# Performance work log

Measured on AMD Instinct MI355X. Metric: run time of the kernel, lower is better.

The kernel has to match this reference:

```python
import jax, jax.numpy as jnp
import numpy as np

S, I, H = 4096, 2048, 2048


def setup_inputs() -> dict:
    key = jax.random.key(0)
    ks = jax.random.split(key, 7)
    k = 1.0 / np.sqrt(H)  # torch LSTMCell init range (values don't affect math shape)
    x = jax.random.normal(ks[0], (S, I), dtype=jnp.float32)
    W_ih = jax.random.uniform(ks[1], (4 * H, I), minval=-k, maxval=k, dtype=jnp.float32)
    W_hh = jax.random.uniform(ks[2], (4 * H, H), minval=-k, maxval=k, dtype=jnp.float32)
    b_ih = jax.random.uniform(ks[3], (4 * H,), minval=-k, maxval=k, dtype=jnp.float32)
    b_hh = jax.random.uniform(ks[4], (4 * H,), minval=-k, maxval=k, dtype=jnp.float32)
    xav = np.sqrt(2.0 / (1 + H))  # xavier_normal_ std for a (1, H) tensor
    h0 = jax.random.normal(ks[5], (1, H), dtype=jnp.float32) * xav
    c0 = jax.random.normal(ks[6], (1, H), dtype=jnp.float32) * xav
    return {"x": x, "W_ih": W_ih, "W_hh": W_hh, "b_ih": b_ih, "b_hh": b_hh, "h0": h0, "c0": c0}


def reference(x, W_ih, W_hh, b_ih, b_hh, h0, c0):
    # Precompute input contribution for all timesteps in one big GEMM: (S, 4H)
    x_gates = x @ W_ih.T + b_ih + b_hh
    W_hh_T = W_hh.T  # (H, 4H)

    def step(carry, xg_t):
        h, c = carry  # each (H,)
        gates = xg_t + h @ W_hh_T  # (4H,)
        i, f, g, o = jnp.split(gates, 4)
        i = jax.nn.sigmoid(i)
        f = jax.nn.sigmoid(f)
        g = jnp.tanh(g)
        o = jax.nn.sigmoid(o)
        c_new = f * c + i * g
        h_new = o * jnp.tanh(c_new)
        return (h_new, c_new), h_new

    _, hs = jax.lax.scan(step, (h0[0], c0[0]), x_gates)
    return hs[:, None, :]  # (S, 1, H) matching torch.stack of (1, H) states
```

## Files before the change

kernel.cpp:

```cpp
#include <hip/hip_runtime.h>
#include <hip/hip_bf16.h>

#define S_LEN 4096
#define IDIM  2048
#define HDIM  2048
#define G4    8192
#define NB    256
#define TPB   512

__device__ __forceinline__ unsigned short f2bf(float f) {
  unsigned u = __float_as_uint(f);
  unsigned r = (u + 0x7FFFu + ((u >> 16) & 1u)) >> 16;
  return (unsigned short)r;
}
__device__ __forceinline__ float bf2f(unsigned short h) {
  return __uint_as_float(((unsigned)h) << 16);
}

__device__ __forceinline__ unsigned long long pack_rec(float h, unsigned tag) {
  return (unsigned long long)__float_as_uint(h) | ((unsigned long long)tag << 32);
}

#define TS 64
#define KS 16
__global__ __launch_bounds__(256) void gemm_xg(
    const float* __restrict__ x, const float* __restrict__ Wih,
    const float* __restrict__ bih, const float* __restrict__ bhh,
    unsigned short* __restrict__ xg) {
  __shared__ float At[KS][TS + 4];
  __shared__ float Bt[KS][TS + 4];
  const int t  = threadIdx.x;
  const int tx = t & 15, ty = t >> 4;
  const int s0 = blockIdx.y * TS, j0 = blockIdx.x * TS;
  const int lrow = t >> 2, lk4 = (t & 3) * 4;
  float acc[4][4] = {};

  for (int k0 = 0; k0 < IDIM; k0 += KS) {
    const float4 av = *(const float4*)&x  [(size_t)(s0 + lrow) * IDIM + k0 + lk4];
    const float4 bv = *(const float4*)&Wih[(size_t)(j0 + lrow) * IDIM + k0 + lk4];
    __syncthreads();
    At[lk4+0][lrow] = av.x; At[lk4+1][lrow] = av.y;
    At[lk4+2][lrow] = av.z; At[lk4+3][lrow] = av.w;
    Bt[lk4+0][lrow] = bv.x; Bt[lk4+1][lrow] = bv.y;
    Bt[lk4+2][lrow] = bv.z; Bt[lk4+3][lrow] = bv.w;
    __syncthreads();
#pragma unroll
    for (int k = 0; k < KS; ++k) {
      float a[4], bb[4];
      *(float4*)a  = *(const float4*)&At[k][ty * 4];
      *(float4*)bb = *(const float4*)&Bt[k][tx * 4];
#pragma unroll
      for (int i = 0; i < 4; ++i)
#pragma unroll
        for (int j = 0; j < 4; ++j)
          acc[i][j] = fmaf(a[i], bb[j], acc[i][j]);
    }
  }
  const float4 b1 = *(const float4*)&bih[j0 + tx * 4];
  const float4 b2 = *(const float4*)&bhh[j0 + tx * 4];
  const float bias[4] = {b1.x + b2.x, b1.y + b2.y, b1.z + b2.z, b1.w + b2.w};
#pragma unroll
  for (int i = 0; i < 4; ++i) {
    ushort4 pk;
    pk.x = f2bf(acc[i][0] + bias[0]);
    pk.y = f2bf(acc[i][1] + bias[1]);
    pk.z = f2bf(acc[i][2] + bias[2]);
    pk.w = f2bf(acc[i][3] + bias[3]);
    *(ushort4*)&xg[(size_t)(s0 + ty * 4 + i) * G4 + j0 + tx * 4] = pk;
  }
}

__global__ __launch_bounds__(TPB, 2) void lstm_scan(
    const unsigned short* __restrict__ xg, const float* __restrict__ Whh,
    const float* __restrict__ h0, const float* __restrict__ c0,
    float* __restrict__ out, unsigned long long* __restrict__ rec) {
  __shared__ float h_sh[2][HDIM];
  __shared__ float part[16][33];

  const int b = blockIdx.x, t = threadIdx.x;
  const int r = t & 31, c = t >> 5;
  const size_t row_g = (size_t)(r >> 3) * HDIM + b * 8 + (r & 7);

  float w[128];
  {
    const float* wp = Whh + row_g * HDIM + c * 128;
#pragma unroll
    for (int i = 0; i < 32; ++i) {
      const float4 v = *(const float4*)(wp + i * 4);
      w[i*4+0] = v.x; w[i*4+1] = v.y; w[i*4+2] = v.z; w[i*4+3] = v.w;
    }
  }
  float c_reg = (t < 8) ? c0[b * 8 + t] : 0.f;

  for (int ts = 0; ts < S_LEN; ++ts) {
    const int buf = ts & 1;
    float xgv = 0.f;
    if (t < 32)
      xgv = bf2f(xg[(size_t)ts * G4 + (size_t)(t >> 3) * HDIM + b * 8 + (t & 7)]);

    if (ts == 0) {
      h_sh[0][t]        = h0[t];
      h_sh[0][t + 512]  = h0[t + 512];
      h_sh[0][t + 1024] = h0[t + 1024];
      h_sh[0][t + 1536] = h0[t + 1536];
    } else {
      const unsigned want = (unsigned)ts;
      const unsigned long long* slot = rec + (size_t)(ts & 1) * HDIM;
      unsigned long long r0, r1, r2, r3;
      for (;;) {
        r0 = __hip_atomic_load(slot + t,        __ATOMIC_RELAXED, __HIP_MEMORY_SCOPE_AGENT);
        r1 = __hip_atomic_load(slot + t + 512,  __ATOMIC_RELAXED, __HIP_MEMORY_SCOPE_AGENT);
        r2 = __hip_atomic_load(slot + t + 1024, __ATOMIC_RELAXED, __HIP_MEMORY_SCOPE_AGENT);
        r3 = __hip_atomic_load(slot + t + 1536, __ATOMIC_RELAXED, __HIP_MEMORY_SCOPE_AGENT);
        if ((unsigned)(r0 >> 32) == want && (unsigned)(r1 >> 32) == want &&
            (unsigned)(r2 >> 32) == want && (unsigned)(r3 >> 32) == want)
          break;
        __builtin_amdgcn_s_sleep(2);
      }
      h_sh[buf][t]        = __uint_as_float((unsigned)r0);
      h_sh[buf][t + 512]  = __uint_as_float((unsigned)r1);
      h_sh[buf][t + 1024] = __uint_as_float((unsigned)r2);
      h_sh[buf][t + 1536] = __uint_as_float((unsigned)r3);
    }
    __syncthreads();

    float acc = 0.f;
    const float4* h4 = (const float4*)&h_sh[buf][c * 128];
#pragma unroll
    for (int i = 0; i < 32; ++i) {
      const float4 hv = h4[i];
      acc = fmaf(w[i*4+0], hv.x, acc);
      acc = fmaf(w[i*4+1], hv.y, acc);
      acc = fmaf(w[i*4+2], hv.z, acc);
      acc = fmaf(w[i*4+3], hv.w, acc);
    }
    part[c][r] = acc;
    __syncthreads();

    if (t < 64) {
      float gval = 0.f;
      if (t < 32) {
        float s = xgv;
#pragma unroll
        for (int i = 0; i < 16; ++i) s += part[i][t];
        gval = ((t >> 3) == 2) ? tanhf(s) : 1.f / (1.f + __expf(-s));
      }
      const float iv = __shfl(gval, (t & 7));
      const float fv = __shfl(gval, (t & 7) + 8);
      const float gv = __shfl(gval, (t & 7) + 16);
      const float ov = __shfl(gval, (t & 7) + 24);
      if (t < 8) {
        c_reg = fmaf(fv, c_reg, iv * gv);
        const float hn = ov * tanhf(c_reg);
        const int j = b * 8 + t;
        out[(size_t)ts * HDIM + j] = hn;
        __hip_atomic_store(&rec[(size_t)((ts + 1) & 1) * HDIM + j],
                           pack_rec(hn, (unsigned)(ts + 1)),
                           __ATOMIC_RELAXED, __HIP_MEMORY_SCOPE_AGENT);
      }
    }
  }
}

extern "C" void kernel_launch(void* const* d_in, const int* in_sizes, int n_in,
                              void* d_out, int out_size, void* d_ws, size_t ws_size,
                              hipStream_t stream) {
  const float* x   = (const float*)d_in[0];
  const float* Wih = (const float*)d_in[1];
  const float* Whh = (const float*)d_in[2];
  const float* bih = (const float*)d_in[3];
  const float* bhh = (const float*)d_in[4];
  const float* h0  = (const float*)d_in[5];
  const float* c0  = (const float*)d_in[6];
  float* out = (float*)d_out;

  unsigned long long* rec = (unsigned long long*)d_ws;
  unsigned short* xg = (unsigned short*)((char*)d_ws + 32768);

  hipMemsetAsync(rec, 0, 2 * HDIM * sizeof(unsigned long long), stream);

  dim3 g1(G4 / TS, S_LEN / TS);
  gemm_xg<<<g1, 256, 0, stream>>>(x, Wih, bih, bhh, xg);

  void* args[] = {(void*)&xg, (void*)&Whh, (void*)&h0,
                  (void*)&c0, (void*)&out, (void*)&rec};
  hipLaunchCooperativeKernel((void*)lstm_scan, dim3(NB), dim3(TPB),
                             args, 0, stream);
}
```

Before: 13.41 ms.

## Use bf16 MFMA for input GEMM and warp-per-unit recurrent scan

```diff
diff --git a/kernel.cpp b/kernel.cpp
--- a/kernel.cpp
+++ b/kernel.cpp
@@ -8,6 +8,9 @@
 #define NB    256
 #define TPB   512
 
+typedef __attribute__((ext_vector_type(8))) short     bf16x8;
+typedef __attribute__((ext_vector_type(4))) float     f32x4;
+
 __device__ __forceinline__ unsigned short f2bf(float f) {
   unsigned u = __float_as_uint(f);
   unsigned r = (u + 0x7FFFu + ((u >> 16) & 1u)) >> 16;
@@ -16,57 +19,88 @@
 __device__ __forceinline__ float bf2f(unsigned short h) {
   return __uint_as_float(((unsigned)h) << 16);
 }
-
 __device__ __forceinline__ unsigned long long pack_rec(float h, unsigned tag) {
   return (unsigned long long)__float_as_uint(h) | ((unsigned long long)tag << 32);
 }
 
-#define TS 64
-#define KS 16
-__global__ __launch_bounds__(256) void gemm_xg(
+#define BM 128
+#define BKK 32
+#define LDK 40
+
+__global__ __launch_bounds__(256) void gemm_xg_mfma(
     const float* __restrict__ x, const float* __restrict__ Wih,
     const float* __restrict__ bih, const float* __restrict__ bhh,
     unsigned short* __restrict__ xg) {
-  __shared__ float At[KS][TS + 4];
-  __shared__ float Bt[KS][TS + 4];
-  const int t  = threadIdx.x;
-  const int tx = t & 15, ty = t >> 4;
-  const int s0 = blockIdx.y * TS, j0 = blockIdx.x * TS;
-  const int lrow = t >> 2, lk4 = (t & 3) * 4;
-  float acc[4][4] = {};
-
-  for (int k0 = 0; k0 < IDIM; k0 += KS) {
-    const float4 av = *(const float4*)&x  [(size_t)(s0 + lrow) * IDIM + k0 + lk4];
-    const float4 bv = *(const float4*)&Wih[(size_t)(j0 + lrow) * IDIM + k0 + lk4];
+  __shared__ unsigned short As[BM][LDK];
+  __shared__ unsigned short Bs[BM][LDK];
+
+  const int t = threadIdx.x;
+  const int lane = t & 63, wid = t >> 6;
+  const int wr = wid >> 1, wc = wid & 1;
+
+  int bid = ((int)blockIdx.x & 7) * 256 + ((int)blockIdx.x >> 3);
+  const int s0 = (bid >> 6) * BM;
+  const int j0 = (bid & 63) * BM;
+
+  f32x4 acc[4][4] = {};
+
+  float bias[4];
+#pragma unroll
+  for (int n = 0; n < 4; ++n) {
+    const int col = j0 + wc * 64 + n * 16 + (lane & 15);
+    bias[n] = bih[col] + bhh[col];
+  }
+
+  for (int k0 = 0; k0 < IDIM; k0 += BKK) {
+    float4 va[4], vb[4];
+#pragma unroll
+    for (int u = 0; u < 4; ++u) {
+      const int f = t + 256 * u;
+      const int row = f >> 3, kc = (f & 7) * 4;
+      va[u] = *(const float4*)&x  [(size_t)(s0 + row) * IDIM + k0 + kc];
+      vb[u] = *(const float4*)&Wih[(size_t)(j0 + row) * IDIM + k0 + kc];
+    }
     __syncthreads();
-    At[lk4+0][lrow] = av.x; At[lk4+1][lrow] = av.y;
-    At[lk4+2][lrow] = av.z; At[lk4+3][lrow] = av.w;
-    Bt[lk4+0][lrow] = bv.x; Bt[lk4+1][lrow] = bv.y;
-    Bt[lk4+2][lrow] = bv.z; Bt[lk4+3][lrow] = bv.w;
+#pragma unroll
+    for (int u = 0; u < 4; ++u) {
+      const int f = t + 256 * u;
+      const int row = f >> 3, kc = (f & 7) * 4;
+      ushort4 pa, pb;
+      pa.x = f2bf(va[u].x); pa.y = f2bf(va[u].y);
+      pa.z = f2bf(va[u].z); pa.w = f2bf(va[u].w);
+      pb.x = f2bf(vb[u].x); pb.y = f2bf(vb[u].y);
+      pb.z = f2bf(vb[u].z); pb.w = f2bf(vb[u].w);
+      *(ushort4*)&As[row][kc] = pa;
+      *(ushort4*)&Bs[row][kc] = pb;
+    }
     __syncthreads();
-#pragma unroll
-    for (int k = 0; k < KS; ++k) {
-      float a[4], bb[4];
-      *(float4*)a  = *(const float4*)&At[k][ty * 4];
-      *(float4*)bb = *(const float4*)&Bt[k][tx * 4];
-#pragma unroll
-      for (int i = 0; i < 4; ++i)
-#pragma unroll
-        for (int j = 0; j < 4; ++j)
-          acc[i][j] = fmaf(a[i], bb[j], acc[i][j]);
-    }
-  }
-  const float4 b1 = *(const float4*)&bih[j0 + tx * 4];
-  const float4 b2 = *(const float4*)&bhh[j0 + tx * 4];
-  const float bias[4] = {b1.x + b2.x, b1.y + b2.y, b1.z + b2.z, b1.w + b2.w};
-#pragma unroll
-  for (int i = 0; i < 4; ++i) {
-    ushort4 pk;
-    pk.x = f2bf(acc[i][0] + bias[0]);
-    pk.y = f2bf(acc[i][1] + bias[1]);
-    pk.z = f2bf(acc[i][2] + bias[2]);
-    pk.w = f2bf(acc[i][3] + bias[3]);
-    *(ushort4*)&xg[(size_t)(s0 + ty * 4 + i) * G4 + j0 + tx * 4] = pk;
+
+    const int fr = lane & 15, koff = (lane >> 4) * 8;
+    bf16x8 a[4], bfr[4];
+#pragma unroll
+    for (int m = 0; m < 4; ++m)
+      a[m] = *(const bf16x8*)&As[wr * 64 + m * 16 + fr][koff];
+#pragma unroll
+    for (int n = 0; n < 4; ++n)
+      bfr[n] = *(const bf16x8*)&Bs[wc * 64 + n * 16 + fr][koff];
+#pragma unroll
+    for (int m = 0; m < 4; ++m)
+#pragma unroll
+      for (int n = 0; n < 4; ++n)
+        acc[m][n] = __builtin_amdgcn_mfma_f32_16x16x32_bf16(
+            a[m], bfr[n], acc[m][n], 0, 0, 0);
+  }
+
+#pragma unroll
+  for (int m = 0; m < 4; ++m) {
+    const int row0 = s0 + wr * 64 + m * 16 + (lane >> 4) * 4;
+#pragma unroll
+    for (int n = 0; n < 4; ++n) {
+      const int col = j0 + wc * 64 + n * 16 + (lane & 15);
+#pragma unroll
+      for (int r = 0; r < 4; ++r)
+        xg[(size_t)(row0 + r) * G4 + col] = f2bf(acc[m][n][r] + bias[n]);
+    }
   }
 }
 
@@ -74,90 +108,94 @@
     const unsigned short* __restrict__ xg, const float* __restrict__ Whh,
     const float* __restrict__ h0, const float* __restrict__ c0,
     float* __restrict__ out, unsigned long long* __restrict__ rec) {
-  __shared__ float h_sh[2][HDIM];
-  __shared__ float part[16][33];
+  __shared__ float h_sh[2][2176];
 
   const int b = blockIdx.x, t = threadIdx.x;
-  const int r = t & 31, c = t >> 5;
-  const size_t row_g = (size_t)(r >> 3) * HDIM + b * 8 + (r & 7);
-
-  float w[128];
-  {
-    const float* wp = Whh + row_g * HDIM + c * 128;
-#pragma unroll
-    for (int i = 0; i < 32; ++i) {
+  const int lane = t & 63, wid = t >> 6;
+  const int j = b * 8 + wid;
+
+  float w4[4][32];
+#pragma unroll
+  for (int g = 0; g < 4; ++g) {
+    const float* wp = Whh + ((size_t)g * HDIM + j) * HDIM + lane * 32;
+#pragma unroll
+    for (int i = 0; i < 8; ++i) {
       const float4 v = *(const float4*)(wp + i * 4);
-      w[i*4+0] = v.x; w[i*4+1] = v.y; w[i*4+2] = v.z; w[i*4+3] = v.w;
-    }
-  }
-  float c_reg = (t < 8) ? c0[b * 8 + t] : 0.f;
+      w4[g][i*4+0] = v.x; w4[g][i*4+1] = v.y;
+      w4[g][i*4+2] = v.z; w4[g][i*4+3] = v.w;
+    }
+  }
+  float c_reg = (lane == 0) ? c0[j] : 0.f;
+  const int hbase = lane * 32 + ((lane >> 1) << 2);
 
   for (int ts = 0; ts < S_LEN; ++ts) {
     const int buf = ts & 1;
     float xgv = 0.f;
-    if (t < 32)
-      xgv = bf2f(xg[(size_t)ts * G4 + (size_t)(t >> 3) * HDIM + b * 8 + (t & 7)]);
+    if (lane < 4)
+      xgv = bf2f(xg[(size_t)ts * G4 + (size_t)lane * HDIM + j]);
 
     if (ts == 0) {
-      h_sh[0][t]        = h0[t];
-      h_sh[0][t + 512]  = h0[t + 512];
-      h_sh[0][t + 1024] = h0[t + 1024];
-      h_sh[0][t + 1536] = h0[t + 1536];
+#pragma unroll
+      for (int kk = 0; kk < 4; ++kk) {
+        const int idx = t + kk * 512;
+        h_sh[0][idx + ((idx >> 6) << 2)] = h0[idx];
+      }
     } else {
       const unsigned want = (unsigned)ts;
-      const unsigned long long* slot = rec + (size_t)(ts & 1) * HDIM;
-      unsigned long long r0, r1, r2, r3;
+      const unsigned long long* slot = rec + (size_t)buf * HDIM;
+      unsigned long long r0 = 0, r1 = 0, r2 = 0, r3 = 0;
+      int d0 = 0, d1 = 0, d2 = 0, d3 = 0;
       for (;;) {
-        r0 = __hip_atomic_load(slot + t,        __ATOMIC_RELAXED, __HIP_MEMORY_SCOPE_AGENT);
-        r1 = __hip_atomic_load(slot + t + 512,  __ATOMIC_RELAXED, __HIP_MEMORY_SCOPE_AGENT);
-        r2 = __hip_atomic_load(slot + t + 1024, __ATOMIC_RELAXED, __HIP_MEMORY_SCOPE_AGENT);
-        r3 = __hip_atomic_load(slot + t + 1536, __ATOMIC_RELAXED, __HIP_MEMORY_SCOPE_AGENT);
-        if ((unsigned)(r0 >> 32) == want && (unsigned)(r1 >> 32) == want &&
-            (unsigned)(r2 >> 32) == want && (unsigned)(r3 >> 32) == want)
-          break;
-        __builtin_amdgcn_s_sleep(2);
+        if (!d0) { r0 = __hip_atomic_load(slot + t,        __ATOMIC_RELAXED, __HIP_MEMORY_SCOPE_AGENT); d0 = ((unsigned)(r0 >> 32) == want); }
+        if (!d1) { r1 = __hip_atomic_load(slot + t + 512,  __ATOMIC_RELAXED, __HIP_MEMORY_SCOPE_AGENT); d1 = ((unsigned)(r1 >> 32) == want); }
+        if (!d2) { r2 = __hip_atomic_load(slot + t + 1024, __ATOMIC_RELAXED, __HIP_MEMORY_SCOPE_AGENT); d2 = ((unsigned)(r2 >> 32) == want); }
+        if (!d3) { r3 = __hip_atomic_load(slot + t + 1536, __ATOMIC_RELAXED, __HIP_MEMORY_SCOPE_AGENT); d3 = ((unsigned)(r3 >> 32) == want); }
+        if (d0 & d1 & d2 & d3) break;
+        __builtin_amdgcn_s_sleep(1);
       }
-      h_sh[buf][t]        = __uint_as_float((unsigned)r0);
-      h_sh[buf][t + 512]  = __uint_as_float((unsigned)r1);
-      h_sh[buf][t + 1024] = __uint_as_float((unsigned)r2);
-      h_sh[buf][t + 1536] = __uint_as_float((unsigned)r3);
+      const int i0 = t, i1 = t + 512, i2 = t + 1024, i3 = t + 1536;
+      h_sh[buf][i0 + ((i0 >> 6) << 2)] = __uint_as_float((unsigned)r0);
+      h_sh[buf][i1 + ((i1 >> 6) << 2)] = __uint_as_float((unsigned)r1);
+      h_sh[buf][i2 + ((i2 >> 6) << 2)] = __uint_as_float((unsigned)r2);
+      h_sh[buf][i3 + ((i3 >> 6) << 2)] = __uint_as_float((unsigned)r3);
     }
     __syncthreads();
 
-    float acc = 0.f;
-    const float4* h4 = (const float4*)&h_sh[buf][c * 128];
-#pragma unroll
-    for (int i = 0; i < 32; ++i) {
+    float a0 = 0.f, a1 = 0.f, a2 = 0.f, a3 = 0.f;
+    const float4* h4 = (const float4*)&h_sh[buf][hbase];
+#pragma unroll
+    for (int i = 0; i < 8; ++i) {
       const float4 hv = h4[i];
-      acc = fmaf(w[i*4+0], hv.x, acc);
-      acc = fmaf(w[i*4+1], hv.y, acc);
-      acc = fmaf(w[i*4+2], hv.z, acc);
-      acc = fmaf(w[i*4+3], hv.w, acc);
-    }
-    part[c][r] = acc;
-    __syncthreads();
-
-    if (t < 64) {
-      float gval = 0.f;
-      if (t < 32) {
-        float s = xgv;
-#pragma unroll
-        for (int i = 0; i < 16; ++i) s += part[i][t];
-        gval = ((t >> 3) == 2) ? tanhf(s) : 1.f / (1.f + __expf(-s));
-      }
-      const float iv = __shfl(gval, (t & 7));
-      const float fv = __shfl(gval, (t & 7) + 8);
-      const float gv = __shfl(gval, (t & 7) + 16);
-      const float ov = __shfl(gval, (t & 7) + 24);
-      if (t < 8) {
-        c_reg = fmaf(fv, c_reg, iv * gv);
-        const float hn = ov * tanhf(c_reg);
-        const int j = b * 8 + t;
-        out[(size_t)ts * HDIM + j] = hn;
-        __hip_atomic_store(&rec[(size_t)((ts + 1) & 1) * HDIM + j],
-                           pack_rec(hn, (unsigned)(ts + 1)),
-                           __ATOMIC_RELAXED, __HIP_MEMORY_SCOPE_AGENT);
-      }
+      a0 = fmaf(w4[0][i*4+0], hv.x, a0); a0 = fmaf(w4[0][i*4+1], hv.y, a0);
+      a0 = fmaf(w4[0][i*4+2], hv.z, a0); a0 = fmaf(w4[0][i*4+3], hv.w, a0);
+      a1 = fmaf(w4[1][i*4+0], hv.x, a1); a1 = fmaf(w4[1][i*4+1], hv.y, a1);
+      a1 = fmaf(w4[1][i*4+2], hv.z, a1); a1 = fmaf(w4[1][i*4+3], hv.w, a1);
+      a2 = fmaf(w4[2][i*4+0], hv.x, a2); a2 = fmaf(w4[2][i*4+1], hv.y, a2);
+      a2 = fmaf(w4[2][i*4+2], hv.z, a2); a2 = fmaf(w4[2][i*4+3], hv.w, a2);
+      a3 = fmaf(w4[3][i*4+0], hv.x, a3); a3 = fmaf(w4[3][i*4+1], hv.y, a3);
+      a3 = fmaf(w4[3][i*4+2], hv.z, a3); a3 = fmaf(w4[3][i*4+3], hv.w, a3);
+    }
+#pragma unroll
+    for (int m = 1; m < 64; m <<= 1) {
+      a0 += __shfl_xor(a0, m);
+      a1 += __shfl_xor(a1, m);
+      a2 += __shfl_xor(a2, m);
+      a3 += __shfl_xor(a3, m);
+    }
+    float sv = (lane == 0) ? a0 : (lane == 1) ? a1 : (lane == 2) ? a2 : a3;
+    sv += xgv;
+    const float av = (lane == 2) ? tanhf(sv) : 1.f / (1.f + __expf(-sv));
+    const float iv = __shfl(av, 0);
+    const float fv = __shfl(av, 1);
+    const float gv = __shfl(av, 2);
+    const float ov = __shfl(av, 3);
+    if (lane == 0) {
+      c_reg = fmaf(fv, c_reg, iv * gv);
+      const float hn = ov * tanhf(c_reg);
+      __hip_atomic_store(&rec[(size_t)(buf ^ 1) * HDIM + j],
+                         pack_rec(hn, (unsigned)(ts + 1)),
+                         __ATOMIC_RELAXED, __HIP_MEMORY_SCOPE_AGENT);
+      out[(size_t)ts * HDIM + j] = hn;
     }
   }
 }
@@ -179,8 +217,7 @@
 
   hipMemsetAsync(rec, 0, 2 * HDIM * sizeof(unsigned long long), stream);
 
-  dim3 g1(G4 / TS, S_LEN / TS);
-  gemm_xg<<<g1, 256, 0, stream>>>(x, Wih, bih, bhh, xg);
+  gemm_xg_mfma<<<dim3(2048), 256, 0, stream>>>(x, Wih, bih, bhh, xg);
 
   void* args[] = {(void*)&xg, (void*)&Whh, (void*)&h0,
                   (void*)&c0, (void*)&out, (void*)&rec};
```

Result: faster. 12.78 ms (-4.7%).
